# Kernel optimization log

Hardware: AMD Instinct MI355X
Metric: run time of the kernel (lower is better)

## Reference

```python
import jax, jax.numpy as jnp
import numpy as np

B, D, H, W = 16, 96, 96, 96
NUM_POINTS = 4096
THRESH = 0.5
CH = [3, 64, 128, 256, 512]   # shared-MLP channel progression (3 mlp layers + global_dim)
GROUPS = 8
EPS = 1e-5
HEAD_HIDDEN = 128


def setup_inputs() -> dict:
    key = jax.random.key(0)
    ks = jax.random.split(key, 8)
    inp = {"volume": jax.random.uniform(ks[0], (B, 1, D, H, W), jnp.float32)}
    for i in range(4):
        # Conv1d(kernel=1, no bias) weight (out, in); kaiming normal fan_out -> std=sqrt(2/out)
        inp[f"w{i+1}"] = jax.random.normal(ks[1 + i], (CH[i + 1], CH[i]), jnp.float32) * np.sqrt(2.0 / CH[i + 1]).astype(np.float32)
        inp[f"gn{i+1}_w"] = jnp.ones((CH[i + 1],), jnp.float32)
        inp[f"gn{i+1}_b"] = jnp.zeros((CH[i + 1],), jnp.float32)
    inp["fc1_w"] = jax.random.normal(ks[5], (HEAD_HIDDEN, CH[-1]), jnp.float32) * np.sqrt(2.0 / HEAD_HIDDEN).astype(np.float32)
    inp["fc1_b"] = jnp.zeros((HEAD_HIDDEN,), jnp.float32)
    inp["fc2_w"] = jax.random.normal(ks[6], (1, HEAD_HIDDEN), jnp.float32) * np.sqrt(2.0).astype(np.float32)
    inp["fc2_b"] = jnp.zeros((1,), jnp.float32)
    return inp


def volume_to_points(volume):
    """Batched, jit-safe version of volume_to_pointcloud (eval mode: linspace sampling)."""
    b, _, d, h, w = volume.shape
    mask = (volume[:, 0] > THRESH).reshape(b, -1)              # (B, D*H*W)
    n = mask.sum(axis=1)                                        # (B,) foreground counts
    # Stable argsort on ~mask puts foreground flat-indices first, in ascending order
    # == torch nonzero() ordering (row-major over D,H,W).
    order = jnp.argsort(jnp.logical_not(mask), axis=1, stable=True)  # (B, D*H*W)
    p = jnp.arange(NUM_POINTS)
    n_f = n.astype(jnp.float32)[:, None]
    # torch.linspace(0, n-1, P).long(): truncation toward zero
    lin = (p[None, :].astype(jnp.float32) * (n_f - 1.0) / (NUM_POINTS - 1)).astype(jnp.int32)
    lin = jnp.clip(lin, 0, jnp.maximum(n[:, None] - 1, 0))
    wrap = p[None, :] % jnp.maximum(n[:, None], 1)              # n < P fallback
    idx = jnp.where(n[:, None] >= NUM_POINTS, lin, wrap)        # (B, P)
    flat = jnp.take_along_axis(order, idx, axis=1)              # (B, P) flat voxel indices
    dd = flat // (h * w)
    hh = (flat // w) % h
    ww = flat % w
    coords = jnp.stack([dd, hh, ww], axis=1).astype(jnp.float32)  # (B, 3, P)
    scale = jnp.array([max(d - 1, 1), max(h - 1, 1), max(w - 1, 1)], jnp.float32)
    pts = coords / scale[None, :, None] * 2.0 - 1.0
    return jnp.where((n > 0)[:, None, None], pts, 0.0)


def group_norm(x, gamma, beta):
    b, c, npts = x.shape
    xg = x.reshape(b, GROUPS, c // GROUPS, npts)
    mu = xg.mean(axis=(2, 3), keepdims=True)
    var = xg.var(axis=(2, 3), keepdims=True)
    xn = ((xg - mu) * jax.lax.rsqrt(var + EPS)).reshape(b, c, npts)
    return xn * gamma[None, :, None] + beta[None, :, None]


def reference(volume, w1, gn1_w, gn1_b, w2, gn2_w, gn2_b, w3, gn3_w, gn3_b,
              w4, gn4_w, gn4_b, fc1_w, fc1_b, fc2_w, fc2_b):
    x = volume_to_points(volume)                                 # (B, 3, P)
    for cw, gw, gb in ((w1, gn1_w, gn1_b), (w2, gn2_w, gn2_b),
                       (w3, gn3_w, gn3_b), (w4, gn4_w, gn4_b)):
        x = jax.nn.relu(group_norm(jnp.einsum('oc,bcn->bon', cw, x), gw, gb))
    g = x.max(axis=2)                                            # (B, 512) global max-pool
    hdn = jax.nn.relu(g @ fc1_w.T + fc1_b)                       # dropout is identity in eval
    logits = (hdn @ fc2_w.T + fc2_b)[:, 0]                       # squeeze(-1) -> (B,)
    return logits
```

## Files before the change

kernel.cpp:

```cpp
#include <hip/hip_runtime.h>
#include <hip/hip_bf16.h>

#define NB 16
#define VOX 884736
#define NPTS 4096
#define CHUNK 1024
#define NCHUNK 864

typedef _Float16 f16x8 __attribute__((ext_vector_type(8)));
typedef _Float16 f16x4 __attribute__((ext_vector_type(4)));
typedef float f32x4 __attribute__((ext_vector_type(4)));


__global__ __launch_bounds__(256) void count_kernel(const float* __restrict__ vol,
                                                    int* __restrict__ counts,
                                                    unsigned long long* __restrict__ bits) {
    int blk = blockIdx.x;
    const float4* v4 = (const float4*)(vol + (size_t)blk * CHUNK);
    float4 v = v4[threadIdx.x];
    int nib = (v.x > 0.5f) | ((v.y > 0.5f) << 1) | ((v.z > 0.5f) << 2) | ((v.w > 0.5f) << 3);
    __shared__ unsigned char nibs[256];
    nibs[threadIdx.x] = (unsigned char)nib;
    int cnt = __popc(nib);
    for (int off = 32; off; off >>= 1) cnt += __shfl_down(cnt, off, 64);
    __shared__ int s[4];
    if ((threadIdx.x & 63) == 0) s[threadIdx.x >> 6] = cnt;
    __syncthreads();
    if (threadIdx.x < 16) {
        unsigned long long wd = 0;
        #pragma unroll
        for (int i = 0; i < 16; i++)
            wd |= (unsigned long long)nibs[threadIdx.x * 16 + i] << (4 * i);
        bits[(size_t)blk * 16 + threadIdx.x] = wd;
    }
    if (threadIdx.x == 0) counts[blk] = s[0] + s[1] + s[2] + s[3];
}

__global__ __launch_bounds__(1024) void scan_kernel(const int* __restrict__ counts,
                                                    int* __restrict__ prefix,
                                                    int* __restrict__ totals) {
    __shared__ int s[1024];
    int b = blockIdx.x, t = threadIdx.x;
    int v = (t < NCHUNK) ? counts[b * NCHUNK + t] : 0;
    s[t] = v;
    __syncthreads();
    for (int off = 1; off < 1024; off <<= 1) {
        int x = (t >= off) ? s[t - off] : 0;
        __syncthreads();
        s[t] += x;
        __syncthreads();
    }
    if (t < NCHUNK) prefix[b * NCHUNK + t] = s[t] - v;
    if (t == NCHUNK - 1) totals[b] = s[t];
}


__global__ __launch_bounds__(256) void points_kernel(const unsigned long long* __restrict__ bits,
                                                     const int* __restrict__ prefix,
                                                     const int* __restrict__ totals,
                                                     const float* __restrict__ w1,
                                                     float* __restrict__ pts,
                                                     float* __restrict__ pstat1) {
    int b = blockIdx.x >> 4;
    int pc = blockIdx.x & 15;
    int p = pc * 256 + threadIdx.x;
    __shared__ int spref[NCHUNK];
    __shared__ float sw1[192];
    for (int i = threadIdx.x; i < NCHUNK; i += 256) spref[i] = prefix[b * NCHUNK + i];
    if (threadIdx.x < 192) sw1[threadIdx.x] = w1[threadIdx.x];
    __syncthreads();
    int n = totals[b];
    float px = 0.f, py = 0.f, pz = 0.f;
    if (n > 0) {
        int k;
        if (n >= NPTS) {
            float t = (float)p * ((float)n - 1.0f);
            t = t / 4095.0f;
            k = (int)t;
            if (k > n - 1) k = n - 1;
            if (k < 0) k = 0;
        } else {
            k = p % n;
        }
        int lo = 0, hi = NCHUNK - 1;
        while (lo < hi) {
            int mid = (lo + hi + 1) >> 1;
            if (spref[mid] <= k) lo = mid; else hi = mid - 1;
        }
        int rr = k - spref[lo];
        const unsigned long long* wb = bits + ((size_t)b * NCHUNK + lo) * 16;
        unsigned long long chosen = 0;
        int wordidx = 0;
        bool found = false;
        #pragma unroll
        for (int w = 0; w < 16; w++) {
            unsigned long long m = wb[w];
            int pcnt = __popcll(m);
            bool take = (!found) && (rr < pcnt);
            if (take) { chosen = m; wordidx = w; found = true; }
            if (!found) rr -= pcnt;
        }
        int pos = 0;
        unsigned long long m64 = chosen;
        int c = __popcll(m64 & 0xFFFFFFFFull);
        if (rr >= c) { pos = 32; rr -= c; m64 >>= 32; }
        unsigned mm = (unsigned)m64;
        c = __popc(mm & 0xFFFFu); if (rr >= c) { pos += 16; rr -= c; mm >>= 16; }
        c = __popc(mm & 0xFFu);   if (rr >= c) { pos += 8;  rr -= c; mm >>= 8; }
        c = __popc(mm & 0xFu);    if (rr >= c) { pos += 4;  rr -= c; mm >>= 4; }
        c = __popc(mm & 0x3u);    if (rr >= c) { pos += 2;  rr -= c; mm >>= 2; }
        c = mm & 1u;              if (rr >= c) { pos += 1; }
        int flat = lo * CHUNK + wordidx * 64 + pos;
        int dd = flat / 9216;
        int rem = flat - dd * 9216;
        int hh = rem / 96;
        int ww = rem - hh * 96;
        px = (float)dd / 95.0f * 2.0f - 1.0f;
        py = (float)hh / 95.0f * 2.0f - 1.0f;
        pz = (float)ww / 95.0f * 2.0f - 1.0f;
    }
    pts[((size_t)b * 3 + 0) * NPTS + p] = px;
    pts[((size_t)b * 3 + 1) * NPTS + p] = py;
    pts[((size_t)b * 3 + 2) * NPTS + p] = pz;
    float s[8] = {}, q[8] = {};
    #pragma unroll
    for (int o = 0; o < 64; o++) {
        float a = sw1[o * 3 + 0] * px + sw1[o * 3 + 1] * py + sw1[o * 3 + 2] * pz;
        s[o >> 3] += a;
        q[o >> 3] += a * a;
    }
    __shared__ float red[4][8][2];
    int wv = threadIdx.x >> 6;
    #pragma unroll
    for (int g = 0; g < 8; g++) {
        float S = s[g], Q = q[g];
        for (int off = 32; off; off >>= 1) {
            S += __shfl_down(S, off, 64);
            Q += __shfl_down(Q, off, 64);
        }
        if ((threadIdx.x & 63) == 0) { red[wv][g][0] = S; red[wv][g][1] = Q; }
    }
    __syncthreads();
    if (threadIdx.x < 8) {
        int g = threadIdx.x;
        float S = red[0][g][0] + red[1][g][0] + red[2][g][0] + red[3][g][0];
        float Q = red[0][g][1] + red[1][g][1] + red[2][g][1] + red[3][g][1];
        float* d = pstat1 + (((size_t)(b * 8 + g)) * 16 + pc) * 2;
        d[0] = S; d[1] = Q;
    }
}

__global__ __launch_bounds__(64) void gn_finalize1(const float* __restrict__ pstat,
                                                   const float* __restrict__ gamma,
                                                   const float* __restrict__ beta,
                                                   float* __restrict__ scale,
                                                   float* __restrict__ shift) {
    int b = blockIdx.x >> 3, g = blockIdx.x & 7;
    const float* base = pstat + (size_t)(b * 8 + g) * 32;
    float S = 0.f, Q = 0.f;
    if (threadIdx.x < 16) { S = base[threadIdx.x * 2]; Q = base[threadIdx.x * 2 + 1]; }
    for (int off = 8; off; off >>= 1) {
        S += __shfl_down(S, off, 64);
        Q += __shfl_down(Q, off, 64);
    }
    __shared__ float ms[2];
    if (threadIdx.x == 0) {
        float inv = 1.0f / (8.0f * 4096.0f);
        float mu = S * inv;
        float var = Q * inv - mu * mu;
        if (var < 0.f) var = 0.f;
        ms[0] = mu; ms[1] = rsqrtf(var + 1e-5f);
    }
    __syncthreads();
    if (threadIdx.x < 8) {
        int c = g * 8 + threadIdx.x;
        float ga = gamma[c] * ms[1];
        scale[b * 64 + c] = ga;
        shift[b * 64 + c] = beta[c] - ms[0] * ga;
    }
}


__global__ __launch_bounds__(256) void norm1(const float* __restrict__ pts,
                                             const float* __restrict__ w1,
                                             const float* __restrict__ scale,
                                             const float* __restrict__ shift,
                                             _Float16* __restrict__ x) {
    int b = blockIdx.x >> 4;
    int pc = blockIdx.x & 15;
    int p = pc * 256 + threadIdx.x;
    __shared__ float sw1[192], ssc[64], ssh[64];
    if (threadIdx.x < 192) sw1[threadIdx.x] = w1[threadIdx.x];
    if (threadIdx.x < 64) {
        ssc[threadIdx.x] = scale[b * 64 + threadIdx.x];
        ssh[threadIdx.x] = shift[b * 64 + threadIdx.x];
    }
    __syncthreads();
    float x0 = pts[((size_t)b * 3 + 0) * NPTS + p];
    float x1 = pts[((size_t)b * 3 + 1) * NPTS + p];
    float x2 = pts[((size_t)b * 3 + 2) * NPTS + p];
    int p16g = (b * NPTS + p) >> 4;
    int pr = p & 15;
    #pragma unroll
    for (int cb = 0; cb < 2; cb++)
        #pragma unroll
        for (int k = 0; k < 4; k++) {
            f16x8 v;
            #pragma unroll
            for (int e = 0; e < 8; e++) {
                int o = cb * 32 + k * 8 + e;
                float a = sw1[o * 3 + 0] * x0 + sw1[o * 3 + 1] * x1 + sw1[o * 3 + 2] * x2;
                v[e] = (_Float16)fmaxf(a * ssc[o] + ssh[o], 0.f);
            }
            *(f16x8*)(x + (((size_t)p16g * 2 + cb) * 64 + k * 16 + pr) * 8) = v;
        }
}


template <int CIN, int COUT>
__global__ __launch_bounds__(256) void cast_w_frag(const float* __restrict__ wf,
                                                   _Float16* __restrict__ wh) {
    constexpr int NCB = CIN / 32;
    constexpr int NCHK = (COUT / 16) * NCB * 64;
    int t = blockIdx.x * 256 + threadIdx.x;
    if (t >= NCHK) return;
    int lane = t & 63;
    int cb = (t >> 6) % NCB;
    int ob = t / (64 * NCB);
    int o = ob * 16 + (lane & 15);
    int c0 = cb * 32 + (lane >> 4) * 8;
    const float* src = wf + (size_t)o * CIN + c0;
    f16x8 v;
    #pragma unroll
    for (int e = 0; e < 8; e++) v[e] = (_Float16)src[e];
    *(f16x8*)(wh + (size_t)t * 8) = v;
}


template <int CIN, int COUT>
__global__ __launch_bounds__(256) void mfma_gemm(const _Float16* __restrict__ xa,
                                                 const _Float16* __restrict__ wf,
                                                 _Float16* __restrict__ y,
                                                 float* __restrict__ pstat) {
    constexpr int NCB = CIN / 32;
    int b = blockIdx.z;
    int wv = threadIdx.x >> 6;
    int lane = threadIdx.x & 63;
    int lr = lane & 15;
    int lk = lane >> 4;
    int P16 = (b * NPTS + blockIdx.x * 256 + wv * 64) >> 4;
    int O16 = blockIdx.y * 4;
    f32x4 acc[4][4] = {};
    #pragma unroll 2
    for (int cb = 0; cb < NCB; cb++) {
        f16x8 af[4], bf[4];
        #pragma unroll
        for (int i = 0; i < 4; i++)
            af[i] = *(const f16x8*)(xa + (((size_t)(P16 + i) * NCB + cb) * 64 + lane) * 8);
        #pragma unroll
        for (int i = 0; i < 4; i++)
            bf[i] = *(const f16x8*)(wf + (((size_t)(O16 + i) * NCB + cb) * 64 + lane) * 8);
        #pragma unroll
        for (int pf = 0; pf < 4; pf++)
            #pragma unroll
            for (int of = 0; of < 4; of++)
                acc[pf][of] = __builtin_amdgcn_mfma_f32_16x16x32_f16(af[pf], bf[of], acc[pf][of], 0, 0, 0);
    }
    int Pblk = (b * NPTS + blockIdx.x * 256 + wv * 64) >> 6;
    _Float16* yt = y + ((size_t)Pblk * (COUT / 64) + blockIdx.y) * 4096;
    #pragma unroll
    for (int of = 0; of < 4; of++)
        #pragma unroll
        for (int pf = 0; pf < 4; pf++) {
            f16x4 v;
            #pragma unroll
            for (int j = 0; j < 4; j++) v[j] = (_Float16)acc[pf][of][j];
            *(f16x4*)(yt + ((size_t)(of * 4 + pf) * 64 + lane) * 4) = v;
        }
    __shared__ float sred[4][64][2];
    #pragma unroll
    for (int of = 0; of < 4; of++) {
        float S = 0.f, Q = 0.f;
        #pragma unroll
        for (int pf = 0; pf < 4; pf++)
            #pragma unroll
            for (int j = 0; j < 4; j++) {
                float v = acc[pf][of][j];
                S += v; Q += v * v;
            }
        S += __shfl_xor(S, 16, 64); Q += __shfl_xor(Q, 16, 64);
        S += __shfl_xor(S, 32, 64); Q += __shfl_xor(Q, 32, 64);
        if (lk == 0) { sred[wv][of * 16 + lr][0] = S; sred[wv][of * 16 + lr][1] = Q; }
    }
    __syncthreads();
    if (threadIdx.x < 64) {
        int o = threadIdx.x;
        float S = sred[0][o][0] + sred[1][o][0] + sred[2][o][0] + sred[3][o][0];
        float Q = sred[0][o][1] + sred[1][o][1] + sred[2][o][1] + sred[3][o][1];
        float* d = pstat + (((size_t)b * COUT + blockIdx.y * 64 + o) * 16 + blockIdx.x) * 2;
        d[0] = S; d[1] = Q;
    }
}


template <int C>
__global__ __launch_bounds__(256) void gn_finalizeG(const float* __restrict__ pstat,
                                                    const float* __restrict__ gamma,
                                                    const float* __restrict__ beta,
                                                    float* __restrict__ scale,
                                                    float* __restrict__ shift) {
    constexpr int GS = C / 8;
    int b = blockIdx.x >> 3, g = blockIdx.x & 7;
    const float* base = pstat + ((size_t)b * C + g * GS) * 32;
    float S = 0.f, Q = 0.f;
    for (int i = threadIdx.x; i < GS * 16; i += 256) { S += base[2 * i]; Q += base[2 * i + 1]; }
    for (int off = 32; off; off >>= 1) {
        S += __shfl_down(S, off, 64);
        Q += __shfl_down(Q, off, 64);
    }
    __shared__ float ss[8];
    if ((threadIdx.x & 63) == 0) {
        ss[(threadIdx.x >> 6) * 2] = S;
        ss[(threadIdx.x >> 6) * 2 + 1] = Q;
    }
    __syncthreads();
    __shared__ float ms[2];
    if (threadIdx.x == 0) {
        float St = ss[0] + ss[2] + ss[4] + ss[6];
        float Qt = ss[1] + ss[3] + ss[5] + ss[7];
        float inv = 1.0f / ((float)GS * 4096.0f);
        float mu = St * inv;
        float var = Qt * inv - mu * mu;
        if (var < 0.f) var = 0.f;
        ms[0] = mu; ms[1] = rsqrtf(var + 1e-5f);
    }
    __syncthreads();
    for (int i = threadIdx.x; i < GS; i += 256) {
        int c = g * GS + i;
        float ga = gamma[c] * ms[1];
        scale[(size_t)b * C + c] = ga;
        shift[(size_t)b * C + c] = beta[c] - ms[0] * ga;
    }
}


template <int C>
__global__ __launch_bounds__(256) void normG(const _Float16* __restrict__ y,
                                             const float* __restrict__ scale,
                                             const float* __restrict__ shift,
                                             _Float16* __restrict__ x) {
    __shared__ _Float16 sl[64 * C];
    int Pblk = blockIdx.x;
    int b = Pblk >> 6;
    const _Float16* yt = y + (size_t)Pblk * 64 * C;
    constexpr int NCH = 64 * C / 4;
    for (int q = threadIdx.x; q < NCH; q += 256) {
        int lane = q & 63;
        int pf = (q >> 6) & 3;
        int of = (q >> 8) & 3;
        int Ob = q >> 10;
        int o = Ob * 64 + of * 16 + (lane & 15);
        int pbase = pf * 16 + (lane >> 4) * 4;
        f16x4 v = *(const f16x4*)(yt + (size_t)q * 4);
        float sc = scale[(size_t)b * C + o];
        float sh = shift[(size_t)b * C + o];
        int ch = o >> 3;
        #pragma unroll
        for (int e = 0; e < 4; e++) {
            int p = pbase + e;
            float r = fmaxf((float)v[e] * sc + sh, 0.f);
            sl[p * C + ((ch ^ (p & 7)) << 3) + (o & 7)] = (_Float16)r;
        }
    }
    __syncthreads();
    int wv = threadIdx.x >> 6;
    int lane = threadIdx.x & 63;
    int p = wv * 16 + (lane & 15);
    int k = lane >> 4;
    int P16 = Pblk * 4 + wv;
    #pragma unroll
    for (int cb = 0; cb < C / 32; cb++) {
        int ch = cb * 4 + k;
        f16x8 v = *(const f16x8*)(sl + p * C + ((ch ^ (p & 7)) << 3));
        *(f16x8*)(x + (((size_t)P16 * (C / 32) + cb) * 64 + lane) * 8) = v;
    }
}


__global__ __launch_bounds__(256) void mfma_gemm_pool(const _Float16* __restrict__ xa,
                                                      const _Float16* __restrict__ wf,
                                                      float* __restrict__ pstat4) {
    constexpr int CIN = 256, NCB = CIN / 32;
    int b = blockIdx.z;
    int wv = threadIdx.x >> 6;
    int lane = threadIdx.x & 63;
    int lr = lane & 15;
    int lk = lane >> 4;
    int P16 = (b * NPTS + blockIdx.x * 256 + wv * 64) >> 4;
    int O16 = blockIdx.y * 4;
    f32x4 acc[4][4] = {};
    #pragma unroll 2
    for (int cb = 0; cb < NCB; cb++) {
        f16x8 af[4], bf[4];
        #pragma unroll
        for (int i = 0; i < 4; i++)
            af[i] = *(const f16x8*)(xa + (((size_t)(P16 + i) * NCB + cb) * 64 + lane) * 8);
        #pragma unroll
        for (int i = 0; i < 4; i++)
            bf[i] = *(const f16x8*)(wf + (((size_t)(O16 + i) * NCB + cb) * 64 + lane) * 8);
        #pragma unroll
        for (int pf = 0; pf < 4; pf++)
            #pragma unroll
            for (int of = 0; of < 4; of++)
                acc[pf][of] = __builtin_amdgcn_mfma_f32_16x16x32_f16(af[pf], bf[of], acc[pf][of], 0, 0, 0);
    }
    __shared__ float sred[4][64][4];
    #pragma unroll
    for (int of = 0; of < 4; of++) {
        float S = 0.f, Q = 0.f, MX = -1e30f, MN = 1e30f;
        #pragma unroll
        for (int pf = 0; pf < 4; pf++)
            #pragma unroll
            for (int j = 0; j < 4; j++) {
                float v = acc[pf][of][j];
                S += v; Q += v * v;
                MX = fmaxf(MX, v); MN = fminf(MN, v);
            }
        S += __shfl_xor(S, 16, 64); Q += __shfl_xor(Q, 16, 64);
        MX = fmaxf(MX, __shfl_xor(MX, 16, 64)); MN = fminf(MN, __shfl_xor(MN, 16, 64));
        S += __shfl_xor(S, 32, 64); Q += __shfl_xor(Q, 32, 64);
        MX = fmaxf(MX, __shfl_xor(MX, 32, 64)); MN = fminf(MN, __shfl_xor(MN, 32, 64));
        if (lk == 0) {
            sred[wv][of * 16 + lr][0] = S;
            sred[wv][of * 16 + lr][1] = Q;
            sred[wv][of * 16 + lr][2] = MX;
            sred[wv][of * 16 + lr][3] = MN;
        }
    }
    __syncthreads();
    if (threadIdx.x < 64) {
        int o = threadIdx.x;
        float S = sred[0][o][0] + sred[1][o][0] + sred[2][o][0] + sred[3][o][0];
        float Q = sred[0][o][1] + sred[1][o][1] + sred[2][o][1] + sred[3][o][1];
        float MX = fmaxf(fmaxf(sred[0][o][2], sred[1][o][2]), fmaxf(sred[2][o][2], sred[3][o][2]));
        float MN = fminf(fminf(sred[0][o][3], sred[1][o][3]), fminf(sred[2][o][3], sred[3][o][3]));
        *(float4*)(pstat4 + (((size_t)b * 512 + blockIdx.y * 64 + o) * 16 + blockIdx.x) * 4) =
            make_float4(S, Q, MX, MN);
    }
}


__global__ __launch_bounds__(256) void pool_final(const float* __restrict__ pstat4,
                                                  const float* __restrict__ gamma,
                                                  const float* __restrict__ beta,
                                                  float* __restrict__ g) {
    int b = blockIdx.x;
    __shared__ float sS[512], sQ[512];
    __shared__ float ms[8][2];
    float Sa[2], Qa[2], MXa[2], MNa[2];
    #pragma unroll
    for (int h = 0; h < 2; h++) {
        int o = threadIdx.x + h * 256;
        float S = 0.f, Q = 0.f, MX = -1e30f, MN = 1e30f;
        for (int pb = 0; pb < 16; pb++) {
            float4 v = *(const float4*)(pstat4 + (((size_t)b * 512 + o) * 16 + pb) * 4);
            S += v.x; Q += v.y; MX = fmaxf(MX, v.z); MN = fminf(MN, v.w);
        }
        Sa[h] = S; Qa[h] = Q; MXa[h] = MX; MNa[h] = MN;
        sS[o] = S; sQ[o] = Q;
    }
    __syncthreads();
    if (threadIdx.x < 8) {
        int gr = threadIdx.x;
        float St = 0.f, Qt = 0.f;
        for (int i = 0; i < 64; i++) { St += sS[gr * 64 + i]; Qt += sQ[gr * 64 + i]; }
        float inv = 1.0f / (64.0f * 4096.0f);
        float mu = St * inv;
        float var = Qt * inv - mu * mu;
        if (var < 0.f) var = 0.f;
        ms[gr][0] = mu; ms[gr][1] = rsqrtf(var + 1e-5f);
    }
    __syncthreads();
    #pragma unroll
    for (int h = 0; h < 2; h++) {
        int o = threadIdx.x + h * 256;
        int gr = o >> 6;
        float sc = gamma[o] * ms[gr][1];
        float sh = beta[o] - ms[gr][0] * sc;
        float m = (sc >= 0.f ? MXa[h] : MNa[h]) * sc + sh;
        g[b * 512 + o] = fmaxf(m, 0.f);
    }
}


__global__ __launch_bounds__(128) void head_kernel(const float* __restrict__ g,
                                                   const float* __restrict__ fc1w,
                                                   const float* __restrict__ fc1b,
                                                   const float* __restrict__ fc2w,
                                                   const float* __restrict__ fc2b,
                                                   float* __restrict__ out) {
    int b = blockIdx.x;
    int o = threadIdx.x;
    __shared__ float sg[512];
    for (int i = threadIdx.x; i < 512; i += 128) sg[i] = g[b * 512 + i];
    __syncthreads();
    float acc = fc1b[o];
    for (int c = 0; c < 512; c++) acc += sg[c] * fc1w[o * 512 + c];
    float h = fmaxf(acc, 0.f) * fc2w[o];
    for (int off = 32; off; off >>= 1) h += __shfl_down(h, off, 64);
    __shared__ float s2[2];
    if ((threadIdx.x & 63) == 0) s2[threadIdx.x >> 6] = h;
    __syncthreads();
    if (threadIdx.x == 0) out[b] = s2[0] + s2[1] + fc2b[0];
}


extern "C" void kernel_launch(void* const* d_in, const int* in_sizes, int n_in,
                              void* d_out, int out_size, void* d_ws, size_t ws_size,
                              hipStream_t stream) {
    const float* vol  = (const float*)d_in[0];
    const float* w1   = (const float*)d_in[1];
    const float* gn1w = (const float*)d_in[2];
    const float* gn1b = (const float*)d_in[3];
    const float* w2   = (const float*)d_in[4];
    const float* gn2w = (const float*)d_in[5];
    const float* gn2b = (const float*)d_in[6];
    const float* w3   = (const float*)d_in[7];
    const float* gn3w = (const float*)d_in[8];
    const float* gn3b = (const float*)d_in[9];
    const float* w4   = (const float*)d_in[10];
    const float* gn4w = (const float*)d_in[11];
    const float* gn4b = (const float*)d_in[12];
    const float* fc1w = (const float*)d_in[13];
    const float* fc1b = (const float*)d_in[14];
    const float* fc2w = (const float*)d_in[15];
    const float* fc2b = (const float*)d_in[16];
    float* out = (float*)d_out;

    char* ws = (char*)d_ws;
    size_t cur = 0;
    auto alloc = [&](size_t bytes) -> void* {
        cur = (cur + 255) & ~(size_t)255;
        void* p = ws + cur;
        cur += bytes;
        return p;
    };
    int*      counts  = (int*)alloc((size_t)NB * NCHUNK * 4);
    int*      prefix  = (int*)alloc((size_t)NB * NCHUNK * 4);
    int*      totals  = (int*)alloc(64);
    unsigned long long* bits = (unsigned long long*)alloc((size_t)NB * NCHUNK * 16 * 8);
    float*    pts     = (float*)alloc((size_t)NB * 3 * NPTS * 4);
    float*    gbuf    = (float*)alloc((size_t)NB * 512 * 4);
    float*    pstat1  = (float*)alloc((size_t)NB * 8 * 16 * 2 * 4);
    float*    pstatG  = (float*)alloc((size_t)NB * 512 * 16 * 2 * 4);
    float*    pstat4  = (float*)alloc((size_t)NB * 512 * 16 * 4 * 4);
    float*    scale   = (float*)alloc((size_t)NB * 512 * 4);
    float*    shift   = (float*)alloc((size_t)NB * 512 * 4);
    _Float16* w2f     = (_Float16*)alloc((size_t)128 * 64 * 2);
    _Float16* w3f     = (_Float16*)alloc((size_t)256 * 128 * 2);
    _Float16* w4f     = (_Float16*)alloc((size_t)512 * 256 * 2);
    _Float16* x1      = (_Float16*)alloc((size_t)NB * NPTS * 64 * 2);
    _Float16* y2      = (_Float16*)alloc((size_t)NB * NPTS * 128 * 2);
    _Float16* x2      = (_Float16*)alloc((size_t)NB * NPTS * 128 * 2);
    _Float16* y3      = (_Float16*)alloc((size_t)NB * NPTS * 256 * 2);
    _Float16* x3      = (_Float16*)alloc((size_t)NB * NPTS * 256 * 2);

    count_kernel<<<dim3(NB * NCHUNK), dim3(256), 0, stream>>>(vol, counts, bits);
    scan_kernel<<<dim3(NB), dim3(1024), 0, stream>>>(counts, prefix, totals);
    points_kernel<<<dim3(NB * 16), dim3(256), 0, stream>>>(bits, prefix, totals, w1, pts, pstat1);

    cast_w_frag<64, 128><<<dim3(4), dim3(256), 0, stream>>>(w2, w2f);
    cast_w_frag<128, 256><<<dim3(16), dim3(256), 0, stream>>>(w3, w3f);
    cast_w_frag<256, 512><<<dim3(64), dim3(256), 0, stream>>>(w4, w4f);

    gn_finalize1<<<dim3(NB * 8), dim3(64), 0, stream>>>(pstat1, gn1w, gn1b, scale, shift);
    norm1<<<dim3(NB * 16), dim3(256), 0, stream>>>(pts, w1, scale, shift, x1);

    mfma_gemm<64, 128><<<dim3(16, 2, NB), dim3(256), 0, stream>>>(x1, w2f, y2, pstatG);
    gn_finalizeG<128><<<dim3(NB * 8), dim3(256), 0, stream>>>(pstatG, gn2w, gn2b, scale, shift);
    normG<128><<<dim3(NB * 64), dim3(256), 0, stream>>>(y2, scale, shift, x2);

    mfma_gemm<128, 256><<<dim3(16, 4, NB), dim3(256), 0, stream>>>(x2, w3f, y3, pstatG);
    gn_finalizeG<256><<<dim3(NB * 8), dim3(256), 0, stream>>>(pstatG, gn3w, gn3b, scale, shift);
    normG<256><<<dim3(NB * 64), dim3(256), 0, stream>>>(y3, scale, shift, x3);

    mfma_gemm_pool<<<dim3(16, 8, NB), dim3(256), 0, stream>>>(x3, w4f, pstat4);
    pool_final<<<dim3(NB), dim3(256), 0, stream>>>(pstat4, gn4w, gn4b, gbuf);

    head_kernel<<<dim3(NB), dim3(128), 0, stream>>>(gbuf, fc1w, fc1b, fc2w, fc2b, out);
}
```

Before: 139.4 us.

## Fuse GroupNorm+ReLU prologue into per-point-block MFMA GEMMs and merge weight casts

The separate norm1/normG kernels are removed. Each GEMM block now loads the previous layer's raw output for 64 points, applies scale/shift/ReLU into swizzled LDS, and computes every output channel for those points, skipping the materialised x1/x2/x3 buffers. The three weight-cast launches are merged into one, and partial-stat layouts change to per-64-point blocks with matching finalize loops. In exchange, each block streams the whole weight matrix from global/L2 with one A fragment per wave and a single accumulator per output tile, which reduces MFMA reuse and ILP compared with the previous 4x4 register tiling.

```diff
diff --git a/kernel.cpp b/kernel.cpp
--- a/kernel.cpp
+++ b/kernel.cpp
@@ -181,50 +181,10 @@
 }
 
 
-__global__ __launch_bounds__(256) void norm1(const float* __restrict__ pts,
-                                             const float* __restrict__ w1,
-                                             const float* __restrict__ scale,
-                                             const float* __restrict__ shift,
-                                             _Float16* __restrict__ x) {
-    int b = blockIdx.x >> 4;
-    int pc = blockIdx.x & 15;
-    int p = pc * 256 + threadIdx.x;
-    __shared__ float sw1[192], ssc[64], ssh[64];
-    if (threadIdx.x < 192) sw1[threadIdx.x] = w1[threadIdx.x];
-    if (threadIdx.x < 64) {
-        ssc[threadIdx.x] = scale[b * 64 + threadIdx.x];
-        ssh[threadIdx.x] = shift[b * 64 + threadIdx.x];
-    }
-    __syncthreads();
-    float x0 = pts[((size_t)b * 3 + 0) * NPTS + p];
-    float x1 = pts[((size_t)b * 3 + 1) * NPTS + p];
-    float x2 = pts[((size_t)b * 3 + 2) * NPTS + p];
-    int p16g = (b * NPTS + p) >> 4;
-    int pr = p & 15;
-    #pragma unroll
-    for (int cb = 0; cb < 2; cb++)
-        #pragma unroll
-        for (int k = 0; k < 4; k++) {
-            f16x8 v;
-            #pragma unroll
-            for (int e = 0; e < 8; e++) {
-                int o = cb * 32 + k * 8 + e;
-                float a = sw1[o * 3 + 0] * x0 + sw1[o * 3 + 1] * x1 + sw1[o * 3 + 2] * x2;
-                v[e] = (_Float16)fmaxf(a * ssc[o] + ssh[o], 0.f);
-            }
-            *(f16x8*)(x + (((size_t)p16g * 2 + cb) * 64 + k * 16 + pr) * 8) = v;
-        }
-}
-
-
-template <int CIN, int COUT>
-__global__ __launch_bounds__(256) void cast_w_frag(const float* __restrict__ wf,
-                                                   _Float16* __restrict__ wh) {
-    constexpr int NCB = CIN / 32;
-    constexpr int NCHK = (COUT / 16) * NCB * 64;
-    int t = blockIdx.x * 256 + threadIdx.x;
-    if (t >= NCHK) return;
+__device__ inline void cast_chunk(const float* __restrict__ wf, _Float16* __restrict__ wh,
+                                  int CIN, int t) {
     int lane = t & 63;
+    int NCB = CIN / 32;
     int cb = (t >> 6) % NCB;
     int ob = t / (64 * NCB);
     int o = ob * 16 + (lane & 15);
@@ -236,69 +196,192 @@
     *(f16x8*)(wh + (size_t)t * 8) = v;
 }
 
-
-template <int CIN, int COUT>
-__global__ __launch_bounds__(256) void mfma_gemm(const _Float16* __restrict__ xa,
-                                                 const _Float16* __restrict__ wf,
-                                                 _Float16* __restrict__ y,
-                                                 float* __restrict__ pstat) {
-    constexpr int NCB = CIN / 32;
-    int b = blockIdx.z;
-    int wv = threadIdx.x >> 6;
-    int lane = threadIdx.x & 63;
-    int lr = lane & 15;
-    int lk = lane >> 4;
-    int P16 = (b * NPTS + blockIdx.x * 256 + wv * 64) >> 4;
-    int O16 = blockIdx.y * 4;
-    f32x4 acc[4][4] = {};
+__global__ __launch_bounds__(256) void cast_w_all(const float* __restrict__ w2,
+                                                  const float* __restrict__ w3,
+                                                  const float* __restrict__ w4,
+                                                  _Float16* __restrict__ w2f,
+                                                  _Float16* __restrict__ w3f,
+                                                  _Float16* __restrict__ w4f) {
+    int t = blockIdx.x * 256 + threadIdx.x;
+    if (t < 1024) cast_chunk(w2, w2f, 64, t);
+    else if (t < 1024 + 4096) cast_chunk(w3, w3f, 128, t - 1024);
+    else if (t < 1024 + 4096 + 16384) cast_chunk(w4, w4f, 256, t - 5120);
+}
+
+
+__global__ __launch_bounds__(256) void fused_l2(const float* __restrict__ pts,
+                                                const float* __restrict__ w1,
+                                                const float* __restrict__ scale,
+                                                const float* __restrict__ shift,
+                                                const _Float16* __restrict__ wfrag,
+                                                _Float16* __restrict__ yout,
+                                                float* __restrict__ pstat) {
+    constexpr int CIN = 64, COUT = 128, NCB = 2;
+    __shared__ char smem[8192];
+    __shared__ float sw1[192], ssc[64], ssh[64];
+    _Float16* sl = (_Float16*)smem;
+    float* sred = (float*)smem;
+    int b = blockIdx.y, pblk = blockIdx.x, tid = threadIdx.x;
+    int Pg = b * 64 + pblk;
+    if (tid < 192) sw1[tid] = w1[tid];
+    if (tid < 64) { ssc[tid] = scale[b * 64 + tid]; ssh[tid] = shift[b * 64 + tid]; }
+    __syncthreads();
+    {
+        int p = tid >> 2, qo = (tid & 3) * 16;
+        int pg = pblk * 64 + p;
+        float x0 = pts[((size_t)b * 3 + 0) * NPTS + pg];
+        float x1 = pts[((size_t)b * 3 + 1) * NPTS + pg];
+        float x2 = pts[((size_t)b * 3 + 2) * NPTS + pg];
+        #pragma unroll
+        for (int e = 0; e < 16; e++) {
+            int o = qo + e;
+            float a = sw1[o * 3 + 0] * x0 + sw1[o * 3 + 1] * x1 + sw1[o * 3 + 2] * x2;
+            float r = fmaxf(a * ssc[o] + ssh[o], 0.f);
+            int ch = o >> 3;
+            sl[p * CIN + ((ch ^ (p & 7)) << 3) + (o & 7)] = (_Float16)r;
+        }
+    }
+    __syncthreads();
+    int wv = tid >> 6, lane = tid & 63, lr = lane & 15, lk = lane >> 4;
+    int p = wv * 16 + lr;
+    f16x8 af[NCB];
+    #pragma unroll
+    for (int cb = 0; cb < NCB; cb++) {
+        int ch = cb * 4 + lk;
+        af[cb] = *(const f16x8*)(sl + p * CIN + ((ch ^ (p & 7)) << 3));
+    }
+    __syncthreads();
     #pragma unroll 2
-    for (int cb = 0; cb < NCB; cb++) {
-        f16x8 af[4], bf[4];
-        #pragma unroll
-        for (int i = 0; i < 4; i++)
-            af[i] = *(const f16x8*)(xa + (((size_t)(P16 + i) * NCB + cb) * 64 + lane) * 8);
-        #pragma unroll
-        for (int i = 0; i < 4; i++)
-            bf[i] = *(const f16x8*)(wf + (((size_t)(O16 + i) * NCB + cb) * 64 + lane) * 8);
-        #pragma unroll
-        for (int pf = 0; pf < 4; pf++)
-            #pragma unroll
-            for (int of = 0; of < 4; of++)
-                acc[pf][of] = __builtin_amdgcn_mfma_f32_16x16x32_f16(af[pf], bf[of], acc[pf][of], 0, 0, 0);
-    }
-    int Pblk = (b * NPTS + blockIdx.x * 256 + wv * 64) >> 6;
-    _Float16* yt = y + ((size_t)Pblk * (COUT / 64) + blockIdx.y) * 4096;
-    #pragma unroll
-    for (int of = 0; of < 4; of++)
-        #pragma unroll
-        for (int pf = 0; pf < 4; pf++) {
-            f16x4 v;
-            #pragma unroll
-            for (int j = 0; j < 4; j++) v[j] = (_Float16)acc[pf][of][j];
-            *(f16x4*)(yt + ((size_t)(of * 4 + pf) * 64 + lane) * 4) = v;
-        }
-    __shared__ float sred[4][64][2];
-    #pragma unroll
-    for (int of = 0; of < 4; of++) {
-        float S = 0.f, Q = 0.f;
-        #pragma unroll
-        for (int pf = 0; pf < 4; pf++)
-            #pragma unroll
-            for (int j = 0; j < 4; j++) {
-                float v = acc[pf][of][j];
-                S += v; Q += v * v;
-            }
+    for (int of = 0; of < COUT / 16; of++) {
+        f32x4 acc = {};
+        #pragma unroll
+        for (int cb = 0; cb < NCB; cb++) {
+            f16x8 bf = *(const f16x8*)(wfrag + ((size_t)(of * NCB + cb) * 64 + lane) * 8);
+            acc = __builtin_amdgcn_mfma_f32_16x16x32_f16(af[cb], bf, acc, 0, 0, 0);
+        }
+        f16x4 vv;
+        #pragma unroll
+        for (int j = 0; j < 4; j++) vv[j] = (_Float16)acc[j];
+        *(f16x4*)(yout + ((size_t)Pg * (COUT / 64) + (of >> 2)) * 4096 +
+                  (((of & 3) * 4 + wv) * 64 + lane) * 4) = vv;
+        float S = acc[0] + acc[1] + acc[2] + acc[3];
+        float Q = acc[0] * acc[0] + acc[1] * acc[1] + acc[2] * acc[2] + acc[3] * acc[3];
         S += __shfl_xor(S, 16, 64); Q += __shfl_xor(Q, 16, 64);
         S += __shfl_xor(S, 32, 64); Q += __shfl_xor(Q, 32, 64);
-        if (lk == 0) { sred[wv][of * 16 + lr][0] = S; sred[wv][of * 16 + lr][1] = Q; }
-    }
-    __syncthreads();
-    if (threadIdx.x < 64) {
-        int o = threadIdx.x;
-        float S = sred[0][o][0] + sred[1][o][0] + sred[2][o][0] + sred[3][o][0];
-        float Q = sred[0][o][1] + sred[1][o][1] + sred[2][o][1] + sred[3][o][1];
-        float* d = pstat + (((size_t)b * COUT + blockIdx.y * 64 + o) * 16 + blockIdx.x) * 2;
+        if (lk == 0) {
+            float* d = sred + ((size_t)(wv * COUT + of * 16 + lr)) * 2;
+            d[0] = S; d[1] = Q;
+        }
+    }
+    __syncthreads();
+    for (int o = tid; o < COUT; o += 256) {
+        float S = 0.f, Q = 0.f;
+        #pragma unroll
+        for (int w = 0; w < 4; w++) {
+            const float* d = sred + ((size_t)(w * COUT + o)) * 2;
+            S += d[0]; Q += d[1];
+        }
+        float* d = pstat + (((size_t)(b * 64 + pblk)) * COUT + o) * 2;
         d[0] = S; d[1] = Q;
+    }
+}
+
+
+template <int CIN, int COUT, bool POOL>
+__global__ __launch_bounds__(256) void fused_layer(const _Float16* __restrict__ yprev,
+                                                   const float* __restrict__ scale,
+                                                   const float* __restrict__ shift,
+                                                   const _Float16* __restrict__ wfrag,
+                                                   _Float16* __restrict__ yout,
+                                                   float* __restrict__ pstat) {
+    constexpr int NCB = CIN / 32;
+    constexpr int NST = POOL ? 4 : 2;
+    constexpr int STAGE_B = 64 * CIN * 2;
+    constexpr int SRED_B = 4 * COUT * NST * 4;
+    constexpr int UNION_B = STAGE_B > SRED_B ? STAGE_B : SRED_B;
+    __shared__ char smem[UNION_B];
+    __shared__ float ssc[CIN], ssh[CIN];
+    _Float16* sl = (_Float16*)smem;
+    float* sred = (float*)smem;
+    int b = blockIdx.y, pblk = blockIdx.x, tid = threadIdx.x;
+    int Pg = b * 64 + pblk;
+    for (int i = tid; i < CIN; i += 256) { ssc[i] = scale[b * CIN + i]; ssh[i] = shift[b * CIN + i]; }
+    __syncthreads();
+    const _Float16* yt = yprev + (size_t)Pg * 64 * CIN;
+    constexpr int NCH4 = 64 * CIN / 4;
+    for (int q = tid; q < NCH4; q += 256) {
+        int lane = q & 63;
+        int pf = (q >> 6) & 3;
+        int ofi = (q >> 8) & 3;
+        int Ob = q >> 10;
+        int o = Ob * 64 + ofi * 16 + (lane & 15);
+        int pbase = pf * 16 + (lane >> 4) * 4;
+        f16x4 v = *(const f16x4*)(yt + (size_t)q * 4);
+        float sc = ssc[o], sh = ssh[o];
+        int ch = o >> 3;
+        #pragma unroll
+        for (int e = 0; e < 4; e++) {
+            int p = pbase + e;
+            float r = fmaxf((float)v[e] * sc + sh, 0.f);
+            sl[p * CIN + ((ch ^ (p & 7)) << 3) + (o & 7)] = (_Float16)r;
+        }
+    }
+    __syncthreads();
+    int wv = tid >> 6, lane = tid & 63, lr = lane & 15, lk = lane >> 4;
+    int p = wv * 16 + lr;
+    f16x8 af[NCB];
+    #pragma unroll
+    for (int cb = 0; cb < NCB; cb++) {
+        int ch = cb * 4 + lk;
+        af[cb] = *(const f16x8*)(sl + p * CIN + ((ch ^ (p & 7)) << 3));
+    }
+    __syncthreads();
+    #pragma unroll 2
+    for (int of = 0; of < COUT / 16; of++) {
+        f32x4 acc = {};
+        #pragma unroll
+        for (int cb = 0; cb < NCB; cb++) {
+            f16x8 bf = *(const f16x8*)(wfrag + ((size_t)(of * NCB + cb) * 64 + lane) * 8);
+            acc = __builtin_amdgcn_mfma_f32_16x16x32_f16(af[cb], bf, acc, 0, 0, 0);
+        }
+        if (!POOL) {
+            f16x4 vv;
+            #pragma unroll
+            for (int j = 0; j < 4; j++) vv[j] = (_Float16)acc[j];
+            *(f16x4*)(yout + ((size_t)Pg * (COUT / 64) + (of >> 2)) * 4096 +
+                      (((of & 3) * 4 + wv) * 64 + lane) * 4) = vv;
+        }
+        float S = acc[0] + acc[1] + acc[2] + acc[3];
+        float Q = acc[0] * acc[0] + acc[1] * acc[1] + acc[2] * acc[2] + acc[3] * acc[3];
+        float MX = 0.f, MN = 0.f;
+        if (POOL) {
+            MX = fmaxf(fmaxf(acc[0], acc[1]), fmaxf(acc[2], acc[3]));
+            MN = fminf(fminf(acc[0], acc[1]), fminf(acc[2], acc[3]));
+        }
+        S += __shfl_xor(S, 16, 64); Q += __shfl_xor(Q, 16, 64);
+        S += __shfl_xor(S, 32, 64); Q += __shfl_xor(Q, 32, 64);
+        if (POOL) {
+            MX = fmaxf(MX, __shfl_xor(MX, 16, 64)); MN = fminf(MN, __shfl_xor(MN, 16, 64));
+            MX = fmaxf(MX, __shfl_xor(MX, 32, 64)); MN = fminf(MN, __shfl_xor(MN, 32, 64));
+        }
+        if (lk == 0) {
+            float* d = sred + ((size_t)(wv * COUT + of * 16 + lr)) * NST;
+            d[0] = S; d[1] = Q;
+            if (POOL) { d[2] = MX; d[3] = MN; }
+        }
+    }
+    __syncthreads();
+    for (int o = tid; o < COUT; o += 256) {
+        float S = 0.f, Q = 0.f, MX = -1e30f, MN = 1e30f;
+        #pragma unroll
+        for (int w = 0; w < 4; w++) {
+            const float* d = sred + ((size_t)(w * COUT + o)) * NST;
+            S += d[0]; Q += d[1];
+            if (POOL) { MX = fmaxf(MX, d[2]); MN = fminf(MN, d[3]); }
+        }
+        float* d = pstat + (((size_t)(b * 64 + pblk)) * COUT + o) * NST;
+        if (POOL) *(float4*)d = make_float4(S, Q, MX, MN);
+        else { d[0] = S; d[1] = Q; }
     }
 }
 
@@ -311,9 +394,14 @@
                                                     float* __restrict__ shift) {
     constexpr int GS = C / 8;
     int b = blockIdx.x >> 3, g = blockIdx.x & 7;
-    const float* base = pstat + ((size_t)b * C + g * GS) * 32;
+    const float* base = pstat + (size_t)b * 64 * C * 2;
     float S = 0.f, Q = 0.f;
-    for (int i = threadIdx.x; i < GS * 16; i += 256) { S += base[2 * i]; Q += base[2 * i + 1]; }
+    for (int i = threadIdx.x; i < 64 * GS; i += 256) {
+        int pb = i / GS;
+        int c = g * GS + (i % GS);
+        const float* d = base + ((size_t)pb * C + c) * 2;
+        S += d[0]; Q += d[1];
+    }
     for (int off = 32; off; off >>= 1) {
         S += __shfl_down(S, off, 64);
         Q += __shfl_down(Q, off, 64);
@@ -344,112 +432,6 @@
 }
 
 
-template <int C>
-__global__ __launch_bounds__(256) void normG(const _Float16* __restrict__ y,
-                                             const float* __restrict__ scale,
-                                             const float* __restrict__ shift,
-                                             _Float16* __restrict__ x) {
-    __shared__ _Float16 sl[64 * C];
-    int Pblk = blockIdx.x;
-    int b = Pblk >> 6;
-    const _Float16* yt = y + (size_t)Pblk * 64 * C;
-    constexpr int NCH = 64 * C / 4;
-    for (int q = threadIdx.x; q < NCH; q += 256) {
-        int lane = q & 63;
-        int pf = (q >> 6) & 3;
-        int of = (q >> 8) & 3;
-        int Ob = q >> 10;
-        int o = Ob * 64 + of * 16 + (lane & 15);
-        int pbase = pf * 16 + (lane >> 4) * 4;
-        f16x4 v = *(const f16x4*)(yt + (size_t)q * 4);
-        float sc = scale[(size_t)b * C + o];
-        float sh = shift[(size_t)b * C + o];
-        int ch = o >> 3;
-        #pragma unroll
-        for (int e = 0; e < 4; e++) {
-            int p = pbase + e;
-            float r = fmaxf((float)v[e] * sc + sh, 0.f);
-            sl[p * C + ((ch ^ (p & 7)) << 3) + (o & 7)] = (_Float16)r;
-        }
-    }
-    __syncthreads();
-    int wv = threadIdx.x >> 6;
-    int lane = threadIdx.x & 63;
-    int p = wv * 16 + (lane & 15);
-    int k = lane >> 4;
-    int P16 = Pblk * 4 + wv;
-    #pragma unroll
-    for (int cb = 0; cb < C / 32; cb++) {
-        int ch = cb * 4 + k;
-        f16x8 v = *(const f16x8*)(sl + p * C + ((ch ^ (p & 7)) << 3));
-        *(f16x8*)(x + (((size_t)P16 * (C / 32) + cb) * 64 + lane) * 8) = v;
-    }
-}
-
-
-__global__ __launch_bounds__(256) void mfma_gemm_pool(const _Float16* __restrict__ xa,
-                                                      const _Float16* __restrict__ wf,
-                                                      float* __restrict__ pstat4) {
-    constexpr int CIN = 256, NCB = CIN / 32;
-    int b = blockIdx.z;
-    int wv = threadIdx.x >> 6;
-    int lane = threadIdx.x & 63;
-    int lr = lane & 15;
-    int lk = lane >> 4;
-    int P16 = (b * NPTS + blockIdx.x * 256 + wv * 64) >> 4;
-    int O16 = blockIdx.y * 4;
-    f32x4 acc[4][4] = {};
-    #pragma unroll 2
-    for (int cb = 0; cb < NCB; cb++) {
-        f16x8 af[4], bf[4];
-        #pragma unroll
-        for (int i = 0; i < 4; i++)
-            af[i] = *(const f16x8*)(xa + (((size_t)(P16 + i) * NCB + cb) * 64 + lane) * 8);
-        #pragma unroll
-        for (int i = 0; i < 4; i++)
-            bf[i] = *(const f16x8*)(wf + (((size_t)(O16 + i) * NCB + cb) * 64 + lane) * 8);
-        #pragma unroll
-        for (int pf = 0; pf < 4; pf++)
-            #pragma unroll
-            for (int of = 0; of < 4; of++)
-                acc[pf][of] = __builtin_amdgcn_mfma_f32_16x16x32_f16(af[pf], bf[of], acc[pf][of], 0, 0, 0);
-    }
-    __shared__ float sred[4][64][4];
-    #pragma unroll
-    for (int of = 0; of < 4; of++) {
-        float S = 0.f, Q = 0.f, MX = -1e30f, MN = 1e30f;
-        #pragma unroll
-        for (int pf = 0; pf < 4; pf++)
-            #pragma unroll
-            for (int j = 0; j < 4; j++) {
-                float v = acc[pf][of][j];
-                S += v; Q += v * v;
-                MX = fmaxf(MX, v); MN = fminf(MN, v);
-            }
-        S += __shfl_xor(S, 16, 64); Q += __shfl_xor(Q, 16, 64);
-        MX = fmaxf(MX, __shfl_xor(MX, 16, 64)); MN = fminf(MN, __shfl_xor(MN, 16, 64));
-        S += __shfl_xor(S, 32, 64); Q += __shfl_xor(Q, 32, 64);
-        MX = fmaxf(MX, __shfl_xor(MX, 32, 64)); MN = fminf(MN, __shfl_xor(MN, 32, 64));
-        if (lk == 0) {
-            sred[wv][of * 16 + lr][0] = S;
-            sred[wv][of * 16 + lr][1] = Q;
-            sred[wv][of * 16 + lr][2] = MX;
-            sred[wv][of * 16 + lr][3] = MN;
-        }
-    }
-    __syncthreads();
-    if (threadIdx.x < 64) {
-        int o = threadIdx.x;
-        float S = sred[0][o][0] + sred[1][o][0] + sred[2][o][0] + sred[3][o][0];
-        float Q = sred[0][o][1] + sred[1][o][1] + sred[2][o][1] + sred[3][o][1];
-        float MX = fmaxf(fmaxf(sred[0][o][2], sred[1][o][2]), fmaxf(sred[2][o][2], sred[3][o][2]));
-        float MN = fminf(fminf(sred[0][o][3], sred[1][o][3]), fminf(sred[2][o][3], sred[3][o][3]));
-        *(float4*)(pstat4 + (((size_t)b * 512 + blockIdx.y * 64 + o) * 16 + blockIdx.x) * 4) =
-            make_float4(S, Q, MX, MN);
-    }
-}
-
-
 __global__ __launch_bounds__(256) void pool_final(const float* __restrict__ pstat4,
                                                   const float* __restrict__ gamma,
                                                   const float* __restrict__ beta,
@@ -457,16 +439,16 @@
     int b = blockIdx.x;
     __shared__ float sS[512], sQ[512];
     __shared__ float ms[8][2];
-    float Sa[2], Qa[2], MXa[2], MNa[2];
+    float MXa[2], MNa[2];
     #pragma unroll
     for (int h = 0; h < 2; h++) {
         int o = threadIdx.x + h * 256;
         float S = 0.f, Q = 0.f, MX = -1e30f, MN = 1e30f;
-        for (int pb = 0; pb < 16; pb++) {
-            float4 v = *(const float4*)(pstat4 + (((size_t)b * 512 + o) * 16 + pb) * 4);
+        for (int pb = 0; pb < 64; pb++) {
+            float4 v = *(const float4*)(pstat4 + (((size_t)(b * 64 + pb)) * 512 + o) * 4);
             S += v.x; Q += v.y; MX = fmaxf(MX, v.z); MN = fminf(MN, v.w);
         }
-        Sa[h] = S; Qa[h] = Q; MXa[h] = MX; MNa[h] = MN;
+        MXa[h] = MX; MNa[h] = MN;
         sS[o] = S; sQ[o] = Q;
     }
     __syncthreads();
@@ -552,40 +534,31 @@
     float*    pts     = (float*)alloc((size_t)NB * 3 * NPTS * 4);
     float*    gbuf    = (float*)alloc((size_t)NB * 512 * 4);
     float*    pstat1  = (float*)alloc((size_t)NB * 8 * 16 * 2 * 4);
-    float*    pstatG  = (float*)alloc((size_t)NB * 512 * 16 * 2 * 4);
-    float*    pstat4  = (float*)alloc((size_t)NB * 512 * 16 * 4 * 4);
+    float*    pstatG  = (float*)alloc((size_t)NB * 64 * 256 * 2 * 4);
+    float*    pstat4  = (float*)alloc((size_t)NB * 64 * 512 * 4 * 4);
     float*    scale   = (float*)alloc((size_t)NB * 512 * 4);
     float*    shift   = (float*)alloc((size_t)NB * 512 * 4);
     _Float16* w2f     = (_Float16*)alloc((size_t)128 * 64 * 2);
     _Float16* w3f     = (_Float16*)alloc((size_t)256 * 128 * 2);
     _Float16* w4f     = (_Float16*)alloc((size_t)512 * 256 * 2);
-    _Float16* x1      = (_Float16*)alloc((size_t)NB * NPTS * 64 * 2);
     _Float16* y2      = (_Float16*)alloc((size_t)NB * NPTS * 128 * 2);
-    _Float16* x2      = (_Float16*)alloc((size_t)NB * NPTS * 128 * 2);
     _Float16* y3      = (_Float16*)alloc((size_t)NB * NPTS * 256 * 2);
-    _Float16* x3      = (_Float16*)alloc((size_t)NB * NPTS * 256 * 2);
 
     count_kernel<<<dim3(NB * NCHUNK), dim3(256), 0, stream>>>(vol, counts, bits);
     scan_kernel<<<dim3(NB), dim3(1024), 0, stream>>>(counts, prefix, totals);
     points_kernel<<<dim3(NB * 16), dim3(256), 0, stream>>>(bits, prefix, totals, w1, pts, pstat1);
 
-    cast_w_frag<64, 128><<<dim3(4), dim3(256), 0, stream>>>(w2, w2f);
-    cast_w_frag<128, 256><<<dim3(16), dim3(256), 0, stream>>>(w3, w3f);
-    cast_w_frag<256, 512><<<dim3(64), dim3(256), 0, stream>>>(w4, w4f);
+    cast_w_all<<<dim3(84), dim3(256), 0, stream>>>(w2, w3, w4, w2f, w3f, w4f);
 
     gn_finalize1<<<dim3(NB * 8), dim3(64), 0, stream>>>(pstat1, gn1w, gn1b, scale, shift);
-    norm1<<<dim3(NB * 16), dim3(256), 0, stream>>>(pts, w1, scale, shift, x1);
-
-    mfma_gemm<64, 128><<<dim3(16, 2, NB), dim3(256), 0, stream>>>(x1, w2f, y2, pstatG);
+    fused_l2<<<dim3(64, NB), dim3(256), 0, stream>>>(pts, w1, scale, shift, w2f, y2, pstatG);
+
     gn_finalizeG<128><<<dim3(NB * 8), dim3(256), 0, stream>>>(pstatG, gn2w, gn2b, scale, shift);
-    normG<128><<<dim3(NB * 64), dim3(256), 0, stream>>>(y2, scale, shift, x2);
-
-    mfma_gemm<128, 256><<<dim3(16, 4, NB), dim3(256), 0, stream>>>(x2, w3f, y3, pstatG);
+    fused_layer<128, 256, false><<<dim3(64, NB), dim3(256), 0, stream>>>(y2, scale, shift, w3f, y3, pstatG);
+
     gn_finalizeG<256><<<dim3(NB * 8), dim3(256), 0, stream>>>(pstatG, gn3w, gn3b, scale, shift);
-    normG<256><<<dim3(NB * 64), dim3(256), 0, stream>>>(y3, scale, shift, x3);
-
-    mfma_gemm_pool<<<dim3(16, 8, NB), dim3(256), 0, stream>>>(x3, w4f, pstat4);
+    fused_layer<256, 512, true><<<dim3(64, NB), dim3(256), 0, stream>>>(y3, scale, shift, w4f, nullptr, pstat4);
+
     pool_final<<<dim3(NB), dim3(256), 0, stream>>>(pstat4, gn4w, gn4b, gbuf);
-
     head_kernel<<<dim3(NB), dim3(128), 0, stream>>>(gbuf, fc1w, fc1b, fc2w, fc2b, out);
 }
```

Result: no change. 139.6 us (+0.2%).
